# Kernel optimization log

Measured on AMD Instinct MI355X. Metric: run time of the kernel, lower is better.

Reference implementation:

```python
import jax, jax.numpy as jnp
import numpy as np

B, S, D, H = 8, 2048, 1024, 1024

def setup_inputs() -> dict:
    key = jax.random.key(0)
    ks = jax.random.split(key, 7)
    s = 1.0 / np.sqrt(D)  # torch Linear default init scale (uniform bound)
    x = jax.random.normal(ks[0], (B, S, D), dtype=jnp.float32)
    Wq = jax.random.uniform(ks[1], (D, H), jnp.float32, -s, s)
    bq = jax.random.uniform(ks[2], (H,), jnp.float32, -s, s)
    Wk = jax.random.uniform(ks[3], (D, H), jnp.float32, -s, s)
    bk = jax.random.uniform(ks[4], (H,), jnp.float32, -s, s)
    Wv = jax.random.uniform(ks[5], (D, H), jnp.float32, -s, s)
    bv = jax.random.uniform(ks[6], (H,), jnp.float32, -s, s)
    return {"x": x, "Wq": Wq, "bq": bq, "Wk": Wk, "bk": bk, "Wv": Wv, "bv": bv}

def reference(x, Wq, bq, Wk, bk, Wv, bv):
    scale = jnp.asarray(H ** 0.5, x.dtype)
    q = jnp.einsum('bsd,dh->bsh', x, Wq) + bq
    k = jnp.einsum('bsd,dh->bsh', x, Wk) + bk
    v = jnp.einsum('bsd,dh->bsh', x, Wv) + bv
    scores = jnp.einsum('bqh,bkh->bqk', q, k) / scale  # [B,S,S]
    probs = jax.nn.softmax(scores, axis=-1)
    return jnp.einsum('bqk,bkh->bqh', probs, v)
```

## Files before the change

kernel.cpp:

```cpp
#include <hip/hip_runtime.h>
#include <hip/hip_bf16.h>
#include <stdint.h>

using bf16 = __hip_bfloat16;
typedef __bf16 bf16x8 __attribute__((ext_vector_type(8)));
typedef float f32x4 __attribute__((ext_vector_type(4)));
typedef unsigned short u16x8 __attribute__((ext_vector_type(8)));

#define GLOAD_LDS16(gp, lp)                                                    \
  __builtin_amdgcn_global_load_lds(                                           \
      (const __attribute__((address_space(1))) void*)(gp),                     \
      (__attribute__((address_space(3))) void*)(lp), 16, 0, 0)

#define WAITCNT_VM(N) asm volatile("s_waitcnt vmcnt(" #N ")" ::: "memory")
#define SB0() __builtin_amdgcn_sched_barrier(0)

__device__ inline void store_out(bf16* p, float v)  { *p = __float2bfloat16(v); }
__device__ inline void store_out(float* p, float v) { *p = v; }

template <typename OUT_T, int BIAS_AXIS, bool NFAST>
__global__ __launch_bounds__(512, 2) void gemm256(
    const bf16* __restrict__ A, const bf16* __restrict__ Bt,
    const float* __restrict__ bias0, const float* __restrict__ bias1,
    OUT_T* __restrict__ out0, OUT_T* __restrict__ out1, int Nsplit,
    int K, int lda, int ldb, int ldc,
    long long sA, long long sB, long long sC, float alpha)
{
    __shared__ __align__(16) bf16 lds[4 * 16384];

    const int Mt = gridDim.x, Nt = gridDim.y;
    const int nwg = Mt * Nt * gridDim.z;
    const int hw  = blockIdx.x + Mt * (blockIdx.y + Nt * blockIdx.z);
    const int lg  = (nwg & 7) ? hw : ((hw & 7) * (nwg >> 3) + (hw >> 3));
    const int per = Mt * Nt;
    const int zt  = lg / per;
    const int rem = lg - zt * per;
    int mt, nt;
    if (NFAST) { mt = rem / Nt; nt = rem - mt * Nt; }
    else       { mt = rem % Mt; nt = rem / Mt; }

    A  += (long long)zt * sA;
    Bt += (long long)zt * sB;
    out0 += (long long)zt * sC;
    if (out1) out1 += (long long)zt * sC;

    const int bm = mt * 256;
    const int bn = nt * 256;
    const int t = threadIdx.x, lane = t & 63, w = t >> 6;
    const int wm = w >> 2, wn = w & 3;
    const int fr = lane & 15, c16 = lane >> 4;

    const bf16* gsrc[4];
    int lbase[4];
    #pragma unroll
    for (int c = 0; c < 4; ++c) {
        const int idx  = w * 128 + (c & 1) * 64 + lane;
        const int slot = idx & 7;
        const int r    = ((idx >> 3) << 1) | (idx & 1);
        const int cc   = (slot ^ (r & 7)) >> 1;
        if (c < 2) {
            gsrc[c]  = A + (long long)(bm + r) * lda + cc * 8;
            lbase[c] = w * 1024 + c * 512;
        } else {
            gsrc[c]  = Bt + (long long)(bn + r) * ldb + cc * 8;
            lbase[c] = 8192 + w * 1024 + (c - 2) * 512;
        }
    }

    const int sw   = ((fr & 7) ^ (c16 << 1)) * 8;
    const int offA = (wm * 64 + (fr >> 1)) * 64 + sw;
    const int offB = 8192 + (wn * 32 + (fr >> 1)) * 64 + sw;

    const int nk = K >> 5;

    auto STAGE4 = [&](int jt) {
        const int buf = (jt & 3) * 16384;
        #pragma unroll
        for (int c = 0; c < 4; ++c)
            GLOAD_LDS16(gsrc[c] + jt * 32, &lds[buf + lbase[c]]);
    };

    STAGE4(0); STAGE4(1); STAGE4(2);
    WAITCNT_VM(8);
    __builtin_amdgcn_s_barrier();

    f32x4 acc[8][4] = {};

    for (int j = 0; j < nk; ++j) {
        const int buf = (j & 3) * 16384;
        SB0();

        bf16x8 af[8], bfv[4];
        #pragma unroll
        for (int m = 0; m < 8; ++m)
            af[m] = *reinterpret_cast<const bf16x8*>(&lds[buf + offA + m * 512]);
        #pragma unroll
        for (int n = 0; n < 4; ++n)
            bfv[n] = *reinterpret_cast<const bf16x8*>(&lds[buf + offB + n * 512]);

        if (j + 3 < nk) STAGE4(j + 3);

        #pragma unroll
        for (int m = 0; m < 8; ++m)
            #pragma unroll
            for (int n = 0; n < 4; ++n)
                acc[m][n] = __builtin_amdgcn_mfma_f32_16x16x32_bf16(
                    af[m], bfv[n], acc[m][n], 0, 0, 0);

        SB0();
        if (j + 3 < nk)      { WAITCNT_VM(8); }
        else if (j + 2 < nk) { WAITCNT_VM(4); }
        else if (j + 1 < nk) { WAITCNT_VM(0); }
        __builtin_amdgcn_s_barrier();
    }

    const int colbase = bn + wn * 64 + fr;
    const int rowbase = bm + wm * 128 + c16 * 4;
    #pragma unroll
    for (int n = 0; n < 4; ++n) {
        const int gc = colbase + n * 16;
        const bool seg0 = gc < Nsplit;
        OUT_T* op = seg0 ? out0 : out1;
        const int col = seg0 ? gc : gc - Nsplit;
        float bcol = 0.0f;
        if (BIAS_AXIS == 0) {
            const float* bp = seg0 ? bias0 : bias1;
            if (bp) bcol = bp[col];
        }
        #pragma unroll
        for (int m = 0; m < 8; ++m) {
            #pragma unroll
            for (int jj = 0; jj < 4; ++jj) {
                const int row = rowbase + m * 16 + jj;
                float v = acc[m][n][jj] * alpha;
                if (BIAS_AXIS == 0) v += bcol;
                else if (bias0)     v += bias0[row];
                store_out(&op[(long long)row * ldc + col], v);
            }
        }
    }
}

__global__ __launch_bounds__(256) void f32_to_bf16(
    const float* __restrict__ in, bf16* __restrict__ out, long long n)
{
    long long i = ((long long)blockIdx.x * 256 + threadIdx.x) * 4;
    const long long stride = (long long)gridDim.x * 256 * 4;
    for (; i < n; i += stride) {
        float4 v = *reinterpret_cast<const float4*>(in + i);
        unsigned ux = __float_as_uint(v.x), uy = __float_as_uint(v.y);
        unsigned uz = __float_as_uint(v.z), uw = __float_as_uint(v.w);
        ushort4 o;
        o.x = (unsigned short)((ux + 0x7fffu + ((ux >> 16) & 1u)) >> 16);
        o.y = (unsigned short)((uy + 0x7fffu + ((uy >> 16) & 1u)) >> 16);
        o.z = (unsigned short)((uz + 0x7fffu + ((uz >> 16) & 1u)) >> 16);
        o.w = (unsigned short)((uw + 0x7fffu + ((uw >> 16) & 1u)) >> 16);
        *reinterpret_cast<ushort4*>(out + i) = o;
    }
}

__global__ void transpose_f32_bf16(const float* __restrict__ in,
                                   bf16* __restrict__ out, int R, int C)
{
    __shared__ float tile[32][33];
    const int c0 = blockIdx.x * 32, r0 = blockIdx.y * 32;
    const int tx = threadIdx.x, ty = threadIdx.y;
    #pragma unroll
    for (int i = ty; i < 32; i += 8)
        tile[i][tx] = in[(long long)(r0 + i) * C + (c0 + tx)];
    __syncthreads();
    #pragma unroll
    for (int i = ty; i < 32; i += 8)
        out[(long long)(c0 + i) * R + (r0 + tx)] = __float2bfloat16(tile[tx][i]);
}

__global__ __launch_bounds__(256) void softmax_rows(bf16* __restrict__ Sbuf, int cols)
{
    __shared__ float red[8];
    bf16* p = Sbuf + (long long)blockIdx.x * cols;
    const int t = threadIdx.x;

    u16x8 v = *reinterpret_cast<const u16x8*>(p + t * 8);
    float f[8];
    #pragma unroll
    for (int i = 0; i < 8; ++i)
        f[i] = __uint_as_float((unsigned)v[i] << 16);

    float m = -3.0e38f;
    #pragma unroll
    for (int i = 0; i < 8; ++i) m = fmaxf(m, f[i]);
    #pragma unroll
    for (int o = 32; o; o >>= 1) m = fmaxf(m, __shfl_xor(m, o));
    if ((t & 63) == 0) red[t >> 6] = m;
    __syncthreads();
    m = fmaxf(fmaxf(red[0], red[1]), fmaxf(red[2], red[3]));

    float s = 0.0f;
    #pragma unroll
    for (int i = 0; i < 8; ++i) { f[i] = __expf(f[i] - m); s += f[i]; }
    #pragma unroll
    for (int o = 32; o; o >>= 1) s += __shfl_xor(s, o);
    __syncthreads();
    if ((t & 63) == 0) red[4 + (t >> 6)] = s;
    __syncthreads();
    s = (red[4] + red[5]) + (red[6] + red[7]);
    const float inv = 1.0f / s;

    u16x8 o16;
    #pragma unroll
    for (int i = 0; i < 8; ++i) {
        unsigned u = __float_as_uint(f[i] * inv);
        o16[i] = (unsigned short)((u + 0x7fffu + ((u >> 16) & 1u)) >> 16);
    }
    *reinterpret_cast<u16x8*>(p + t * 8) = o16;
}

extern "C" void kernel_launch(void* const* d_in, const int* in_sizes, int n_in,
                              void* d_out, int out_size, void* d_ws, size_t ws_size,
                              hipStream_t stream)
{
    const int B = 8, S = 2048, D = 1024, H = 1024;
    const float* x  = (const float*)d_in[0];
    const float* Wq = (const float*)d_in[1];
    const float* bq = (const float*)d_in[2];
    const float* Wk = (const float*)d_in[3];
    const float* bk = (const float*)d_in[4];
    const float* Wv = (const float*)d_in[5];
    const float* bv = (const float*)d_in[6];
    float* out = (float*)d_out;

    const size_t nQKV = (size_t)B * S * H;
    const size_t nW   = (size_t)D * H;
    const long long sSH = (long long)S * H;
    const long long sSS = (long long)S * S;

    dim3 tb(32, 8), g256(256), g512(512);
    const float inv_scale = 1.0f / 32.0f;

    bf16* xb   = (bf16*)d_ws;
    bf16* Q    = xb  + nQKV;
    bf16* Kb   = Q   + nQKV;
    bf16* Vt   = Kb  + nQKV;
    bf16* WtQK = Vt  + nQKV;
    bf16* Wtv  = WtQK + 2 * nW;
    bf16* Sc   = Wtv + nW;

    const size_t tierA = (4 * nQKV + 3 * nW + (size_t)B * S * S) * 2;
    const size_t tierB = (4 * nQKV + 3 * nW + (size_t)S * S) * 2;
    const bool bigA = ws_size >= tierA;
    if (ws_size < tierB) return;

    f32_to_bf16<<<dim3(2048), g256, 0, stream>>>(x, xb, (long long)nQKV);
    transpose_f32_bf16<<<dim3(H / 32, D / 32), tb, 0, stream>>>(Wq, WtQK, D, H);
    transpose_f32_bf16<<<dim3(H / 32, D / 32), tb, 0, stream>>>(Wk, WtQK + nW, D, H);
    transpose_f32_bf16<<<dim3(H / 32, D / 32), tb, 0, stream>>>(Wv, Wtv, D, H);

    gemm256<bf16, 0, true><<<dim3(B * S / 256, 2 * H / 256, 1), g512, 0, stream>>>(
        xb, WtQK, bq, bk, Q, Kb, H, D, D, D, H, 0, 0, 0, 1.0f);

    gemm256<bf16, 1, false><<<dim3(H / 256, B * S / 256, 1), g512, 0, stream>>>(
        Wtv, xb, bv, nullptr, Vt, nullptr, 1 << 30, D, D, D, B * S, 0, 0, 0, 1.0f);

    if (bigA) {
        gemm256<bf16, 0, true><<<dim3(S / 256, S / 256, B), g512, 0, stream>>>(
            Q, Kb, nullptr, nullptr, Sc, nullptr, 1 << 30, H, H, H, S,
            sSH, sSH, sSS, inv_scale);
        softmax_rows<<<dim3(B * S), g256, 0, stream>>>(Sc, S);
        gemm256<float, 0, true><<<dim3(S / 256, H / 256, B), g512, 0, stream>>>(
            Sc, Vt, nullptr, nullptr, out, nullptr, 1 << 30, S, S, B * S, H,
            sSS, (long long)S, sSH, 1.0f);
    } else {
        for (int b = 0; b < B; ++b) {
            gemm256<bf16, 0, true><<<dim3(S / 256, S / 256, 1), g512, 0, stream>>>(
                Q + (size_t)b * sSH, Kb + (size_t)b * sSH, nullptr, nullptr,
                Sc, nullptr, 1 << 30, H, H, H, S, 0, 0, 0, inv_scale);
            softmax_rows<<<dim3(S), g256, 0, stream>>>(Sc, S);
            gemm256<float, 0, true><<<dim3(S / 256, H / 256, 1), g512, 0, stream>>>(
                Sc, Vt + (size_t)b * S, nullptr, nullptr,
                out + (size_t)b * sSH, nullptr, 1 << 30, S, S, B * S, H,
                0, 0, 0, 1.0f);
        }
    }
}
```

Measured before the change: 338.8 us.

## Shrink GEMM tiles to 256x128 with 4 waves and triple-buffered LDS

The GEMM kernel moves from a 256x256 tile with 8 waves and a 4-stage LDS ring to a 256x128 tile with 4 waves and a 3-stage ring of about 72KB. Staging, the LDS swizzle and the fragment offsets are reworked for the new layout, and every launch grid doubles along N. The aim is more workgroups for better CU fill and lower LDS use per block. In exchange, each tile reuses its loaded data less and the prefetch depth is shallower.

```diff
diff --git a/kernel.cpp b/kernel.cpp
--- a/kernel.cpp
+++ b/kernel.cpp
@@ -19,14 +19,14 @@
 __device__ inline void store_out(float* p, float v) { *p = v; }
 
 template <typename OUT_T, int BIAS_AXIS, bool NFAST>
-__global__ __launch_bounds__(512, 2) void gemm256(
+__global__ __launch_bounds__(256, 2) void gemm_bm(
     const bf16* __restrict__ A, const bf16* __restrict__ Bt,
     const float* __restrict__ bias0, const float* __restrict__ bias1,
     OUT_T* __restrict__ out0, OUT_T* __restrict__ out1, int Nsplit,
     int K, int lda, int ldb, int ldc,
     long long sA, long long sB, long long sC, float alpha)
 {
-    __shared__ __align__(16) bf16 lds[4 * 16384];
+    __shared__ __align__(16) bf16 lds[36864];
 
     const int Mt = gridDim.x, Nt = gridDim.y;
     const int nwg = Mt * Nt * gridDim.z;
@@ -45,60 +45,63 @@
     if (out1) out1 += (long long)zt * sC;
 
     const int bm = mt * 256;
-    const int bn = nt * 256;
+    const int bn = nt * 128;
     const int t = threadIdx.x, lane = t & 63, w = t >> 6;
-    const int wm = w >> 2, wn = w & 3;
+    const int wm = w >> 1, wn = w & 1;
     const int fr = lane & 15, c16 = lane >> 4;
 
-    const bf16* gsrc[4];
-    int lbase[4];
-    #pragma unroll
-    for (int c = 0; c < 4; ++c) {
-        const int idx  = w * 128 + (c & 1) * 64 + lane;
-        const int slot = idx & 7;
-        const int r    = ((idx >> 3) << 1) | (idx & 1);
-        const int cc   = (slot ^ (r & 7)) >> 1;
-        if (c < 2) {
-            gsrc[c]  = A + (long long)(bm + r) * lda + cc * 8;
-            lbase[c] = w * 1024 + c * 512;
-        } else {
-            gsrc[c]  = Bt + (long long)(bn + r) * ldb + cc * 8;
-            lbase[c] = 8192 + w * 1024 + (c - 2) * 512;
-        }
-    }
-
-    const int sw   = ((fr & 7) ^ (c16 << 1)) * 8;
-    const int offA = (wm * 64 + (fr >> 1)) * 64 + sw;
-    const int offB = 8192 + (wn * 32 + (fr >> 1)) * 64 + sw;
+    const bf16* gA[4];
+    const bf16* gB[2];
+    #pragma unroll
+    for (int k = 0; k < 4; ++k) {
+        const int idx = t + 256 * k, r = idx >> 2, c = idx & 3;
+        gA[k] = A + (long long)(bm + r) * lda + ((c ^ ((r >> 1) & 3)) << 3);
+    }
+    #pragma unroll
+    for (int k = 0; k < 2; ++k) {
+        const int idx = t + 256 * k, r = idx >> 2, c = idx & 3;
+        gB[k] = Bt + (long long)(bn + r) * ldb + ((c ^ ((r >> 1) & 3)) << 3);
+    }
+    const int dstA = t * 8;
+    const int dstB = 8192 + t * 8;
+
+#define STAGE(JT, SLOTB) do {                                                  \
+    GLOAD_LDS16(gA[0] + (JT) * 32, &lds[(SLOTB) + dstA]);                      \
+    GLOAD_LDS16(gA[1] + (JT) * 32, &lds[(SLOTB) + dstA + 2048]);               \
+    GLOAD_LDS16(gA[2] + (JT) * 32, &lds[(SLOTB) + dstA + 4096]);               \
+    GLOAD_LDS16(gA[3] + (JT) * 32, &lds[(SLOTB) + dstA + 6144]);               \
+    GLOAD_LDS16(gB[0] + (JT) * 32, &lds[(SLOTB) + dstB]);                      \
+    GLOAD_LDS16(gB[1] + (JT) * 32, &lds[(SLOTB) + dstB + 2048]);               \
+} while (0)
+
+    const int swz8 = (c16 ^ ((fr >> 1) & 3)) << 3;
+    const int offA = (wm * 128 + fr) * 32 + swz8;
+    const int offB = 8192 + (wn * 64 + fr) * 32 + swz8;
 
     const int nk = K >> 5;
 
-    auto STAGE4 = [&](int jt) {
-        const int buf = (jt & 3) * 16384;
-        #pragma unroll
-        for (int c = 0; c < 4; ++c)
-            GLOAD_LDS16(gsrc[c] + jt * 32, &lds[buf + lbase[c]]);
-    };
-
-    STAGE4(0); STAGE4(1); STAGE4(2);
-    WAITCNT_VM(8);
+    STAGE(0, 0); STAGE(1, 12288);
+    WAITCNT_VM(6);
     __builtin_amdgcn_s_barrier();
 
     f32x4 acc[8][4] = {};
 
+    int slotb = 0;
     for (int j = 0; j < nk; ++j) {
-        const int buf = (j & 3) * 16384;
         SB0();
 
         bf16x8 af[8], bfv[4];
         #pragma unroll
         for (int m = 0; m < 8; ++m)
-            af[m] = *reinterpret_cast<const bf16x8*>(&lds[buf + offA + m * 512]);
+            af[m] = *reinterpret_cast<const bf16x8*>(&lds[slotb + offA + m * 512]);
         #pragma unroll
         for (int n = 0; n < 4; ++n)
-            bfv[n] = *reinterpret_cast<const bf16x8*>(&lds[buf + offB + n * 512]);
-
-        if (j + 3 < nk) STAGE4(j + 3);
+            bfv[n] = *reinterpret_cast<const bf16x8*>(&lds[slotb + offB + n * 512]);
+
+        if (j + 2 < nk) {
+            int s2 = slotb + 24576; if (s2 >= 36864) s2 -= 36864;
+            STAGE(j + 2, s2);
+        }
 
         #pragma unroll
         for (int m = 0; m < 8; ++m)
@@ -108,10 +111,11 @@
                     af[m], bfv[n], acc[m][n], 0, 0, 0);
 
         SB0();
-        if (j + 3 < nk)      { WAITCNT_VM(8); }
-        else if (j + 2 < nk) { WAITCNT_VM(4); }
+        if (j + 2 < nk)      { WAITCNT_VM(6); }
         else if (j + 1 < nk) { WAITCNT_VM(0); }
         __builtin_amdgcn_s_barrier();
+
+        slotb += 12288; if (slotb == 36864) slotb = 0;
     }
 
     const int colbase = bn + wn * 64 + fr;
@@ -139,6 +143,7 @@
             }
         }
     }
+#undef STAGE
 }
 
 __global__ __launch_bounds__(256) void f32_to_bf16(
@@ -234,7 +239,7 @@
     const long long sSH = (long long)S * H;
     const long long sSS = (long long)S * S;
 
-    dim3 tb(32, 8), g256(256), g512(512);
+    dim3 tb(32, 8), g256(256);
     const float inv_scale = 1.0f / 32.0f;
 
     bf16* xb   = (bf16*)d_ws;
@@ -255,27 +260,27 @@
     transpose_f32_bf16<<<dim3(H / 32, D / 32), tb, 0, stream>>>(Wk, WtQK + nW, D, H);
     transpose_f32_bf16<<<dim3(H / 32, D / 32), tb, 0, stream>>>(Wv, Wtv, D, H);
 
-    gemm256<bf16, 0, true><<<dim3(B * S / 256, 2 * H / 256, 1), g512, 0, stream>>>(
+    gemm_bm<bf16, 0, true><<<dim3(B * S / 256, 2 * H / 128, 1), g256, 0, stream>>>(
         xb, WtQK, bq, bk, Q, Kb, H, D, D, D, H, 0, 0, 0, 1.0f);
 
-    gemm256<bf16, 1, false><<<dim3(H / 256, B * S / 256, 1), g512, 0, stream>>>(
+    gemm_bm<bf16, 1, false><<<dim3(H / 256, B * S / 128, 1), g256, 0, stream>>>(
         Wtv, xb, bv, nullptr, Vt, nullptr, 1 << 30, D, D, D, B * S, 0, 0, 0, 1.0f);
 
     if (bigA) {
-        gemm256<bf16, 0, true><<<dim3(S / 256, S / 256, B), g512, 0, stream>>>(
+        gemm_bm<bf16, 0, true><<<dim3(S / 256, S / 128, B), g256, 0, stream>>>(
             Q, Kb, nullptr, nullptr, Sc, nullptr, 1 << 30, H, H, H, S,
             sSH, sSH, sSS, inv_scale);
         softmax_rows<<<dim3(B * S), g256, 0, stream>>>(Sc, S);
-        gemm256<float, 0, true><<<dim3(S / 256, H / 256, B), g512, 0, stream>>>(
+        gemm_bm<float, 0, true><<<dim3(S / 256, H / 128, B), g256, 0, stream>>>(
             Sc, Vt, nullptr, nullptr, out, nullptr, 1 << 30, S, S, B * S, H,
             sSS, (long long)S, sSH, 1.0f);
     } else {
         for (int b = 0; b < B; ++b) {
-            gemm256<bf16, 0, true><<<dim3(S / 256, S / 256, 1), g512, 0, stream>>>(
+            gemm_bm<bf16, 0, true><<<dim3(S / 256, S / 128, 1), g256, 0, stream>>>(
                 Q + (size_t)b * sSH, Kb + (size_t)b * sSH, nullptr, nullptr,
                 Sc, nullptr, 1 << 30, H, H, H, S, 0, 0, 0, inv_scale);
             softmax_rows<<<dim3(S), g256, 0, stream>>>(Sc, S);
-            gemm256<float, 0, true><<<dim3(S / 256, H / 256, 1), g512, 0, stream>>>(
+            gemm_bm<float, 0, true><<<dim3(S / 256, H / 128, 1), g256, 0, stream>>>(
                 Sc, Vt + (size_t)b * S, nullptr, nullptr,
                 out + (size_t)b * sSH, nullptr, 1 << 30, S, S, B * S, H,
                 0, 0, 0, 1.0f);
```

After: 330.6 us. 2.4% less time.
